# Optimization experiments

Measured on AMD Instinct MI355X. Metric: run time of the kernel, lower is better.

The kernel has to match this reference:

```python
import jax, jax.numpy as jnp
import numpy as np

TOP_K = 8
N_GROUPS = 8
TOP_K_GROUPS = 4
ROUTE_SCALE = 2.5


def setup_inputs() -> dict:
    key = jax.random.key(0)
    k1, k2, k3 = jax.random.split(key, 3)
    x = jax.random.normal(k1, (8192, 7168), dtype=jnp.float32)
    weight = jax.random.normal(k2, (256, 7168), dtype=jnp.float32) * 0.02
    bias = jax.random.normal(k3, (256,), dtype=jnp.float32) * 0.1
    return {"x": x, "weight": weight, "bias": bias}


def reference(x, weight, bias):
    n_tokens = x.shape[0]
    n_experts = weight.shape[0]
    # scores: [T, E]
    logits = jnp.einsum('td,ed->te', x, weight)
    scores = jax.nn.sigmoid(logits)
    original_scores = scores
    scores_b = scores + bias  # bias branch (dim == 7168)
    # group-limited routing
    sg = scores_b.reshape(n_tokens, N_GROUPS, n_experts // N_GROUPS)
    # bias is not None -> group score = sum of top-2 within group
    top2, _ = jax.lax.top_k(sg, 2)
    group_scores = top2.sum(axis=-1)  # [T, G]
    _, group_idx = jax.lax.top_k(group_scores, TOP_K_GROUPS)  # [T, Kg]
    keep = jnp.zeros((n_tokens, N_GROUPS), dtype=bool)
    keep = keep.at[jnp.arange(n_tokens)[:, None], group_idx].set(True)
    masked = jnp.where(keep[:, :, None], sg, -jnp.inf).reshape(n_tokens, n_experts)
    # global top-k over masked scores
    _, indices = jax.lax.top_k(masked, TOP_K)  # [T, K]
    weights = jnp.take_along_axis(original_scores, indices, axis=1)
    weights = weights / weights.sum(axis=-1, keepdims=True)  # sigmoid normalization
    weights = weights * ROUTE_SCALE
    return weights.astype(x.dtype), indices
```

## Files before the change

kernel.cpp:

```cpp
#include <hip/hip_runtime.h>
#include <math.h>

#define T_TOKENS 8192
#define NEXP 256
#define DIM 7168
#define NSPLIT 4
#define KSPL (DIM / NSPLIT)
#define NITER (KSPL / 32)
#define NEG_INF (-3.0e38f)

typedef _Float16 f16;
typedef _Float16 f16x8 __attribute__((ext_vector_type(8)));
typedef __fp16 h16x2 __attribute__((ext_vector_type(2)));
typedef float f32x4 __attribute__((ext_vector_type(4)));
typedef float f32x16 __attribute__((ext_vector_type(16)));

#define AS1 __attribute__((address_space(1)))
#define AS3 __attribute__((address_space(3)))
typedef const AS1 f16x8* gf16x8p;

#define WTILED_BYTES (2 * NEXP * DIM * 2)
#define PART_OFF WTILED_BYTES
#define UNSCALE 5.9604644775390625e-8f
#define STG 16384

__global__ __launch_bounds__(256) void wconvert(const float* __restrict__ w,
                                                char* __restrict__ wt) {
    const int n = blockIdx.x * 256 + threadIdx.x;
    const int K8 = n % 896;
    const int e = n / 896;
    const f32x4 u0 = *(const f32x4*)(w + (size_t)e * DIM + K8 * 8);
    const f32x4 u1 = *(const f32x4*)(w + (size_t)e * DIM + K8 * 8 + 4);
    float c[8] = {u0[0]*4096.f, u0[1]*4096.f, u0[2]*4096.f, u0[3]*4096.f,
                  u1[0]*4096.f, u1[1]*4096.f, u1[2]*4096.f, u1[3]*4096.f};
    f16x8 h, g;
#pragma unroll
    for (int j = 0; j < 4; ++j) {
        h16x2 hp = __builtin_amdgcn_cvt_pkrtz(c[2*j], c[2*j+1]);
        float r0 = c[2*j]   - (float)hp[0];
        float r1 = c[2*j+1] - (float)hp[1];
        h16x2 gp = __builtin_amdgcn_cvt_pkrtz(r0, r1);
        h[2*j] = (f16)hp[0]; h[2*j+1] = (f16)hp[1];
        g[2*j] = (f16)gp[0]; g[2*j+1] = (f16)gp[1];
    }
    const int T = K8 >> 2;
    const int kk = (K8 >> 1) & 1;
    const int lhi = K8 & 1;
    const int ntg = e >> 5, l31 = e & 31;
    char* base = wt + (size_t)T * 32768 + ntg * 1024 + lhi * 512 + l31 * 16;
    *(f16x8*)(base + (kk * 2 + 0) * 8192) = h;
    *(f16x8*)(base + (kk * 2 + 1) * 8192) = g;
}

__global__ __launch_bounds__(512, 2) void gemm32r(
    const float* __restrict__ x, const char* __restrict__ wt,
    float* __restrict__ part) {
    __shared__ char smem[3 * STG];
    const int tid = threadIdx.x;
    const int lane = tid & 63;
    const int wcn = tid >> 6;
    const int b = blockIdx.x;
    const int xcd = b & 7;
    const int bz = xcd >> 1;
    const int bm = (xcd & 1) * 32 + (b >> 3);
    const int l31 = lane & 31, lhi = lane >> 5;

    const char* xc = (const char*)x;

    int aoff[2], ldsA[2];
#pragma unroll
    for (int i = 0; i < 2; ++i) {
        const int u = wcn * 2 + i;
        const int ra = u * 8 + (lane >> 3);
        const int ua = lane & 7;
        aoff[i] = (bm * 128 + ra) * (DIM * 4) + bz * (KSPL * 4)
                + ((ua ^ (ra & 7)) * 16);
        ldsA[i] = u * 1024;
    }
    const AS1 char* wq = (const AS1 char*)(wt + (size_t)bz * NITER * 32768
                                           + wcn * 1024 + lane * 16);

    const int swz = l31 & 7;
    int rbase[4], rx[2][2];
#pragma unroll
    for (int mt = 0; mt < 4; ++mt) rbase[mt] = (mt * 32 + l31) * 128;
#pragma unroll
    for (int kk = 0; kk < 2; ++kk)
#pragma unroll
        for (int i = 0; i < 2; ++i)
            rx[kk][i] = ((kk * 4 + lhi * 2 + i) ^ swz) * 16;

    f32x16 acc[4];
#pragma unroll
    for (int mt = 0; mt < 4; ++mt)
#pragma unroll
        for (int r = 0; r < 16; ++r) acc[mt][r] = 0.0f;

    f16x8 wA[2][2], wB[2][2];

#define COMPUTE(CB, W)                                                          \
    {                                                                           \
        _Pragma("unroll")                                                       \
        for (int kk = 0; kk < 2; ++kk) {                                        \
            _Pragma("unroll")                                                   \
            for (int mt = 0; mt < 4; ++mt) {                                    \
                const f32x4 v0 = *(const f32x4*)(smem + (CB) + rbase[mt] + rx[kk][0]); \
                const f32x4 v1 = *(const f32x4*)(smem + (CB) + rbase[mt] + rx[kk][1]); \
                float c[8] = {v0[0]*4096.f, v0[1]*4096.f, v0[2]*4096.f, v0[3]*4096.f,\
                              v1[0]*4096.f, v1[1]*4096.f, v1[2]*4096.f, v1[3]*4096.f};\
                f16x8 a0, a1;                                                   \
                _Pragma("unroll")                                               \
                for (int j = 0; j < 4; ++j) {                                   \
                    h16x2 hp = __builtin_amdgcn_cvt_pkrtz(c[2*j], c[2*j+1]);    \
                    float r0 = c[2*j]   - (float)hp[0];                         \
                    float r1 = c[2*j+1] - (float)hp[1];                         \
                    h16x2 gp = __builtin_amdgcn_cvt_pkrtz(r0, r1);              \
                    a0[2*j] = (f16)hp[0]; a0[2*j+1] = (f16)hp[1];               \
                    a1[2*j] = (f16)gp[0]; a1[2*j+1] = (f16)gp[1];               \
                }                                                               \
                __builtin_amdgcn_s_setprio(1);                                  \
                acc[mt] = __builtin_amdgcn_mfma_f32_32x32x16_f16(a0, W[kk][0], acc[mt], 0, 0, 0); \
                acc[mt] = __builtin_amdgcn_mfma_f32_32x32x16_f16(a1, W[kk][0], acc[mt], 0, 0, 0); \
                acc[mt] = __builtin_amdgcn_mfma_f32_32x32x16_f16(a0, W[kk][1], acc[mt], 0, 0, 0); \
                acc[mt] = __builtin_amdgcn_mfma_f32_32x32x16_f16(a1, W[kk][1], acc[mt], 0, 0, 0); \
                __builtin_amdgcn_s_setprio(0);                                  \
            }                                                                   \
        }                                                                       \
    }

#define BODY(T, WCUR, WNXT)                                                     \
    {                                                                           \
        const int kstage = ((T) + 2 < NITER) ? (T) + 2 : 0;                     \
        _Pragma("unroll")                                                       \
        for (int i = 0; i < 2; ++i)                                             \
            __builtin_amdgcn_global_load_lds(                                   \
                (const AS1 void*)(xc + aoff[i] + kstage * 128),                 \
                (AS3 void*)(smem + nb + ldsA[i]), 16, 0, 0);                    \
        const int kw = ((T) + 1 < NITER) ? (T) + 1 : 0;                         \
        _Pragma("unroll")                                                       \
        for (int kk = 0; kk < 2; ++kk)                                          \
            _Pragma("unroll")                                                   \
            for (int p = 0; p < 2; ++p)                                         \
                WNXT[kk][p] = *(gf16x8p)(wq + (size_t)kw * 32768 + (kk * 2 + p) * 8192); \
        asm volatile("s_waitcnt vmcnt(6)" ::: "memory");                        \
        __builtin_amdgcn_sched_barrier(0);                                      \
        __builtin_amdgcn_s_barrier();                                           \
        COMPUTE(cb, WCUR);                                                      \
        __builtin_amdgcn_s_barrier();                                           \
        const int ob = cb; cb = (cb == 2 * STG) ? 0 : cb + STG; nb = ob;        \
    }

#pragma unroll
    for (int i = 0; i < 2; ++i)
        __builtin_amdgcn_global_load_lds((const AS1 void*)(xc + aoff[i]),
                                         (AS3 void*)(smem + ldsA[i]), 16, 0, 0);
#pragma unroll
    for (int i = 0; i < 2; ++i)
        __builtin_amdgcn_global_load_lds((const AS1 void*)(xc + aoff[i] + 128),
                                         (AS3 void*)(smem + STG + ldsA[i]), 16, 0, 0);
#pragma unroll
    for (int kk = 0; kk < 2; ++kk)
#pragma unroll
        for (int p = 0; p < 2; ++p)
            wA[kk][p] = *(gf16x8p)(wq + (kk * 2 + p) * 8192);

    int cb = 0, nb = 2 * STG;
    for (int tt = 0; tt < NITER; tt += 2) {
        BODY(tt, wA, wB);
        BODY(tt + 1, wB, wA);
    }
#undef BODY
#undef COMPUTE

    float* P = part + (size_t)bz * T_TOKENS * NEXP;
    const int gcol = wcn * 32 + l31;
#pragma unroll
    for (int mt = 0; mt < 4; ++mt)
#pragma unroll
        for (int r = 0; r < 16; ++r) {
            const int row32 = (r & 3) + 8 * (r >> 2) + 4 * lhi;
            const int grow = bm * 128 + mt * 32 + row32;
            P[(size_t)grow * NEXP + gcol] = acc[mt][r];
        }
}

__global__ __launch_bounds__(256) void routing_kernel(const float* __restrict__ part,
                                                      const float* __restrict__ bias,
                                                      float* __restrict__ out) {
    const int lane = threadIdx.x & 63;
    const int t = blockIdx.x * 4 + (threadIdx.x >> 6);

    f32x4 z = {0.f, 0.f, 0.f, 0.f};
#pragma unroll
    for (int s = 0; s < NSPLIT; ++s) {
        const f32x4 v = *((const f32x4*)(part + ((size_t)s * T_TOKENS + t) * NEXP) + lane);
        z[0] += v[0]; z[1] += v[1]; z[2] += v[2]; z[3] += v[3];
    }
    const float s0 = 1.0f / (1.0f + expf(-z[0] * UNSCALE));
    const float s1 = 1.0f / (1.0f + expf(-z[1] * UNSCALE));
    const float s2 = 1.0f / (1.0f + expf(-z[2] * UNSCALE));
    const float s3 = 1.0f / (1.0f + expf(-z[3] * UNSCALE));
    const f32x4 bv = *((const f32x4*)bias + lane);
    float sb0 = s0 + bv[0], sb1 = s1 + bv[1], sb2 = s2 + bv[2], sb3 = s3 + bv[3];

    float m1, m2;
    m1 = sb0; m2 = NEG_INF;
    if (sb1 > m1) { m2 = m1; m1 = sb1; } else if (sb1 > m2) m2 = sb1;
    if (sb2 > m1) { m2 = m1; m1 = sb2; } else if (sb2 > m2) m2 = sb2;
    if (sb3 > m1) { m2 = m1; m1 = sb3; } else if (sb3 > m2) m2 = sb3;
#pragma unroll
    for (int off = 1; off < 8; off <<= 1) {
        const float om1 = __shfl_xor(m1, off);
        const float om2 = __shfl_xor(m2, off);
        const float hi = fmaxf(m1, om1);
        const float lo = fminf(m1, om1);
        m2 = fmaxf(lo, fmaxf(m2, om2));
        m1 = hi;
    }
    const float gs = m1 + m2;

    const float g0 = __shfl(gs, 0),  g1 = __shfl(gs, 8),  g2 = __shfl(gs, 16), g3 = __shfl(gs, 24);
    const float g4 = __shfl(gs, 32), g5 = __shfl(gs, 40), g6 = __shfl(gs, 48), g7 = __shfl(gs, 56);

    float t1 = NEG_INF, t2 = NEG_INF, t3 = NEG_INF, t4 = NEG_INF;
    int i1 = 0, i2 = 0, i3 = 0, i4 = 0;
#define INS4(v, gi)                                                         \
    {                                                                       \
        if (v > t1)      { t4=t3;i4=i3; t3=t2;i3=i2; t2=t1;i2=i1; t1=v;i1=gi; } \
        else if (v > t2) { t4=t3;i4=i3; t3=t2;i3=i2; t2=v;i2=gi; }          \
        else if (v > t3) { t4=t3;i4=i3; t3=v;i3=gi; }                       \
        else if (v > t4) { t4=v;i4=gi; }                                    \
    }
    INS4(g0, 0) INS4(g1, 1) INS4(g2, 2) INS4(g3, 3)
    INS4(g4, 4) INS4(g5, 5) INS4(g6, 6) INS4(g7, 7)
#undef INS4
    const int keepmask = (1 << i1) | (1 << i2) | (1 << i3) | (1 << i4);

    const int g = lane >> 3;
    if (!((keepmask >> g) & 1)) { sb0 = NEG_INF; sb1 = NEG_INF; sb2 = NEG_INF; sb3 = NEG_INF; }

    float wval[8];
    int wi[8];
    float wsum = 0.0f;
#pragma unroll
    for (int r = 0; r < 8; r++) {
        float bvv = sb0;
        int bii = (lane << 2);
        if (sb1 > bvv) { bvv = sb1; bii = (lane << 2) | 1; }
        if (sb2 > bvv) { bvv = sb2; bii = (lane << 2) | 2; }
        if (sb3 > bvv) { bvv = sb3; bii = (lane << 2) | 3; }
#pragma unroll
        for (int off = 1; off < 64; off <<= 1) {
            const float ov = __shfl_xor(bvv, off);
            const int oi = __shfl_xor(bii, off);
            if (ov > bvv || (ov == bvv && oi < bii)) { bvv = ov; bii = oi; }
        }
        const int sl = bii & 3;
        const float cand = (sl == 0) ? s0 : (sl == 1) ? s1 : (sl == 2) ? s2 : s3;
        const float ow = __shfl(cand, bii >> 2);
        wval[r] = ow;
        wi[r] = bii;
        wsum += ow;
        if ((bii >> 2) == lane) {
            if (sl == 0) sb0 = NEG_INF;
            else if (sl == 1) sb1 = NEG_INF;
            else if (sl == 2) sb2 = NEG_INF;
            else sb3 = NEG_INF;
        }
    }
    const float scale = 2.5f / wsum;
    if (lane == 0) {
        float* ow8 = out + (size_t)t * 8;
        float* oi8 = out + (size_t)T_TOKENS * 8 + (size_t)t * 8;
#pragma unroll
        for (int r = 0; r < 8; r++) {
            ow8[r] = wval[r] * scale;
            oi8[r] = (float)wi[r];
        }
    }
}

extern "C" void kernel_launch(void* const* d_in, const int* in_sizes, int n_in,
                              void* d_out, int out_size, void* d_ws, size_t ws_size,
                              hipStream_t stream) {
    const float* x = (const float*)d_in[0];
    const float* w = (const float*)d_in[1];
    const float* bias = (const float*)d_in[2];

    char* wt = (char*)d_ws;
    float* part = (float*)((char*)d_ws + PART_OFF);

    wconvert<<<NEXP * DIM / (256 * 8), 256, 0, stream>>>(w, wt);
    gemm32r<<<256, 512, 0, stream>>>(x, wt, part);
    routing_kernel<<<T_TOKENS / 4, 256, 0, stream>>>(part, bias, (float*)d_out);
}
```

Before: 164.8 us.

## Halve GEMM M-tile to 64 rows, double grid, and use fragment-ordered LDS staging

The router GEMM now works on 64-token tiles instead of 128 and launches 512 blocks instead of 256, with launch bounds raised to allow four blocks per CU. The x tile is staged into LDS in a layout already ordered for the MFMA fragments, which removes the XOR swizzle address math. The pipeline is reordered to one barrier per iteration, with the next W and x loads issued after that barrier. This aims for more occupancy and better latency hiding, at the cost of half the weight reuse per block and twice as much W traffic from L2.

Result: slower. 169.8 us (+3.0%).

```diff
diff --git a/kernel.cpp b/kernel.cpp
--- a/kernel.cpp
+++ b/kernel.cpp
@@ -22,7 +22,7 @@
 #define WTILED_BYTES (2 * NEXP * DIM * 2)
 #define PART_OFF WTILED_BYTES
 #define UNSCALE 5.9604644775390625e-8f
-#define STG 16384
+#define STG 8192
 
 __global__ __launch_bounds__(256) void wconvert(const float* __restrict__ w,
                                                 char* __restrict__ wt) {
@@ -52,7 +52,7 @@
     *(f16x8*)(base + (kk * 2 + 1) * 8192) = g;
 }
 
-__global__ __launch_bounds__(512, 2) void gemm32r(
+__global__ __launch_bounds__(512, 4) void gemm_fo(
     const float* __restrict__ x, const char* __restrict__ wt,
     float* __restrict__ part) {
     __shared__ char smem[3 * STG];
@@ -62,50 +62,44 @@
     const int b = blockIdx.x;
     const int xcd = b & 7;
     const int bz = xcd >> 1;
-    const int bm = (xcd & 1) * 32 + (b >> 3);
+    const int bm = (xcd & 1) * 64 + (b >> 3);
     const int l31 = lane & 31, lhi = lane >> 5;
 
     const char* xc = (const char*)x;
 
-    int aoff[2], ldsA[2];
-#pragma unroll
-    for (int i = 0; i < 2; ++i) {
-        const int u = wcn * 2 + i;
-        const int ra = u * 8 + (lane >> 3);
-        const int ua = lane & 7;
-        aoff[i] = (bm * 128 + ra) * (DIM * 4) + bz * (KSPL * 4)
-                + ((ua ^ (ra & 7)) * 16);
-        ldsA[i] = u * 1024;
-    }
+    const int mt_s = wcn >> 2, kk_s = (wcn >> 1) & 1, j_s = wcn & 1;
+    const int aoff = ((bm * 64 + mt_s * 32 + l31) * DIM + bz * KSPL
+                      + kk_s * 16 + lhi * 8 + j_s * 4) * 4;
+    const int ldsA = wcn * 1024;
+
     const AS1 char* wq = (const AS1 char*)(wt + (size_t)bz * NITER * 32768
                                            + wcn * 1024 + lane * 16);
 
-    const int swz = l31 & 7;
-    int rbase[4], rx[2][2];
-#pragma unroll
-    for (int mt = 0; mt < 4; ++mt) rbase[mt] = (mt * 32 + l31) * 128;
-#pragma unroll
-    for (int kk = 0; kk < 2; ++kk)
-#pragma unroll
-        for (int i = 0; i < 2; ++i)
-            rx[kk][i] = ((kk * 4 + lhi * 2 + i) ^ swz) * 16;
-
-    f32x16 acc[4];
-#pragma unroll
-    for (int mt = 0; mt < 4; ++mt)
+    f32x16 acc[2];
+#pragma unroll
+    for (int mt = 0; mt < 2; ++mt)
 #pragma unroll
         for (int r = 0; r < 16; ++r) acc[mt][r] = 0.0f;
 
     f16x8 wA[2][2], wB[2][2];
+
+#define LOAD_W(T, WDST)                                                         \
+    {                                                                           \
+        _Pragma("unroll")                                                       \
+        for (int kk = 0; kk < 2; ++kk)                                          \
+            _Pragma("unroll")                                                   \
+            for (int p = 0; p < 2; ++p)                                         \
+                WDST[kk][p] = *(gf16x8p)(wq + (size_t)(T) * 32768 + (kk * 2 + p) * 8192); \
+    }
 
 #define COMPUTE(CB, W)                                                          \
     {                                                                           \
         _Pragma("unroll")                                                       \
         for (int kk = 0; kk < 2; ++kk) {                                        \
             _Pragma("unroll")                                                   \
-            for (int mt = 0; mt < 4; ++mt) {                                    \
-                const f32x4 v0 = *(const f32x4*)(smem + (CB) + rbase[mt] + rx[kk][0]); \
-                const f32x4 v1 = *(const f32x4*)(smem + (CB) + rbase[mt] + rx[kk][1]); \
+            for (int mt = 0; mt < 2; ++mt) {                                    \
+                const f32x4 v0 = *(const f32x4*)(smem + (CB) + (mt * 4 + kk * 2 + 0) * 1024 + lane * 16); \
+                const f32x4 v1 = *(const f32x4*)(smem + (CB) + (mt * 4 + kk * 2 + 1) * 1024 + lane * 16); \
                 float c[8] = {v0[0]*4096.f, v0[1]*4096.f, v0[2]*4096.f, v0[3]*4096.f,\
                               v1[0]*4096.f, v1[1]*4096.f, v1[2]*4096.f, v1[3]*4096.f};\
                 f16x8 a0, a1;                                                   \
@@ -130,56 +124,43 @@
 
 #define BODY(T, WCUR, WNXT)                                                     \
     {                                                                           \
-        const int kstage = ((T) + 2 < NITER) ? (T) + 2 : 0;                     \
-        _Pragma("unroll")                                                       \
-        for (int i = 0; i < 2; ++i)                                             \
-            __builtin_amdgcn_global_load_lds(                                   \
-                (const AS1 void*)(xc + aoff[i] + kstage * 128),                 \
-                (AS3 void*)(smem + nb + ldsA[i]), 16, 0, 0);                    \
-        const int kw = ((T) + 1 < NITER) ? (T) + 1 : 0;                         \
-        _Pragma("unroll")                                                       \
-        for (int kk = 0; kk < 2; ++kk)                                          \
-            _Pragma("unroll")                                                   \
-            for (int p = 0; p < 2; ++p)                                         \
-                WNXT[kk][p] = *(gf16x8p)(wq + (size_t)kw * 32768 + (kk * 2 + p) * 8192); \
-        asm volatile("s_waitcnt vmcnt(6)" ::: "memory");                        \
+        asm volatile("s_waitcnt vmcnt(1)" ::: "memory");                        \
         __builtin_amdgcn_sched_barrier(0);                                      \
-        __builtin_amdgcn_s_barrier();                                           \
+        __builtin_amdgcn_s_barrier();    \
+        const int tw = ((T) + 1 < NITER) ? (T) + 1 : 0;                         \
+        LOAD_W(tw, WNXT);                                                       \
+        const int ts = ((T) + 2 < NITER) ? (T) + 2 : 0;                         \
+        __builtin_amdgcn_global_load_lds(                                       \
+            (const AS1 void*)(xc + aoff + ts * 128),                            \
+            (AS3 void*)(smem + sb + ldsA), 16, 0, 0);                           \
         COMPUTE(cb, WCUR);                                                      \
-        __builtin_amdgcn_s_barrier();                                           \
-        const int ob = cb; cb = (cb == 2 * STG) ? 0 : cb + STG; nb = ob;        \
-    }
-
-#pragma unroll
-    for (int i = 0; i < 2; ++i)
-        __builtin_amdgcn_global_load_lds((const AS1 void*)(xc + aoff[i]),
-                                         (AS3 void*)(smem + ldsA[i]), 16, 0, 0);
-#pragma unroll
-    for (int i = 0; i < 2; ++i)
-        __builtin_amdgcn_global_load_lds((const AS1 void*)(xc + aoff[i] + 128),
-                                         (AS3 void*)(smem + STG + ldsA[i]), 16, 0, 0);
-#pragma unroll
-    for (int kk = 0; kk < 2; ++kk)
-#pragma unroll
-        for (int p = 0; p < 2; ++p)
-            wA[kk][p] = *(gf16x8p)(wq + (kk * 2 + p) * 8192);
-
-    int cb = 0, nb = 2 * STG;
+        cb = (cb == 2 * STG) ? 0 : cb + STG;                                    \
+        sb = (sb == 2 * STG) ? 0 : sb + STG;                                    \
+    }
+
+    __builtin_amdgcn_global_load_lds((const AS1 void*)(xc + aoff),
+                                     (AS3 void*)(smem + ldsA), 16, 0, 0);
+    LOAD_W(0, wA);
+    __builtin_amdgcn_global_load_lds((const AS1 void*)(xc + aoff + 128),
+                                     (AS3 void*)(smem + STG + ldsA), 16, 0, 0);
+
+    int cb = 0, sb = 2 * STG;
     for (int tt = 0; tt < NITER; tt += 2) {
         BODY(tt, wA, wB);
         BODY(tt + 1, wB, wA);
     }
 #undef BODY
 #undef COMPUTE
+#undef LOAD_W
 
     float* P = part + (size_t)bz * T_TOKENS * NEXP;
     const int gcol = wcn * 32 + l31;
 #pragma unroll
-    for (int mt = 0; mt < 4; ++mt)
+    for (int mt = 0; mt < 2; ++mt)
 #pragma unroll
         for (int r = 0; r < 16; ++r) {
             const int row32 = (r & 3) + 8 * (r >> 2) + 4 * lhi;
-            const int grow = bm * 128 + mt * 32 + row32;
+            const int grow = bm * 64 + mt * 32 + row32;
             P[(size_t)grow * NEXP + gcol] = acc[mt][r];
         }
 }
@@ -291,6 +272,6 @@
     float* part = (float*)((char*)d_ws + PART_OFF);
 
     wconvert<<<NEXP * DIM / (256 * 8), 256, 0, stream>>>(w, wt);
-    gemm32r<<<256, 512, 0, stream>>>(x, wt, part);
+    gemm_fo<<<512, 512, 0, stream>>>(x, wt, part);
     routing_kernel<<<T_TOKENS / 4, 256, 0, stream>>>(part, bias, (float*)d_out);
 }
```
